# Performance work log

Hardware: AMD Instinct MI355X
Metric: run time of the kernel (lower is better)

Reference implementation:

```python
import jax, jax.numpy as jnp
import numpy as np
from jax import lax

B, DIM, DIM_OUT, NH = 8, 512, 512, 8
HD = DIM_OUT // NH          # 64, also the depthwise-conv channel count
SQ, SKV = (1, 1), (2, 2)    # stride_q, stride_kv
PAD = 1                      # kernel 3 -> padding 3//2
SCALE = HD ** -0.5
EPS = 1e-6


def _dw_conv(x, w, stride):
    # x: [N, C, H, W], w: [C, 1, kh, kw]; depthwise conv (groups = C), no bias
    return lax.conv_general_dilated(
        x, w, window_strides=stride, padding=[(PAD, PAD), (PAD, PAD)],
        dimension_numbers=('NCHW', 'OIHW', 'NCHW'),
        feature_group_count=x.shape[1])


def _ln(x, w, b):
    m = jnp.mean(x, -1, keepdims=True)
    v = jnp.var(x, -1, keepdims=True)
    return (x - m) * lax.rsqrt(v + EPS) * w + b


def _pool(t, w, stride, ln_w, ln_b, H, W):
    # t: [B, NH, 1+H*W, HD] with cls token at index 0
    Bn = t.shape[0]
    cls = t[:, :, :1, :]
    body = t[:, :, 1:, :].reshape(Bn * NH, H, W, HD).transpose(0, 3, 1, 2)
    body = _dw_conv(body, w, stride)
    ph, pw = body.shape[2], body.shape[3]
    body = body.reshape(Bn, NH, HD, ph * pw).transpose(0, 1, 3, 2)
    out = jnp.concatenate([cls, body], axis=2)
    return _ln(out, ln_w, ln_b), (ph, pw)


def _rel_bias(r_q4, q_shape, k_shape, rel_pos_h, rel_pos_w):
    # r_q4: [B, NH, q_h*q_w, HD] (cls token stripped)
    q_h, q_w = q_shape
    k_h, k_w = k_shape

    def dist(qs, ks):
        qr, kr = max(ks / qs, 1.0), max(qs / ks, 1.0)
        d = np.arange(qs)[:, None] * qr - np.arange(ks)[None, :] * kr + (ks - 1) * kr
        return d.astype(np.int64)

    Rh = rel_pos_h[dist(q_h, k_h)]  # [q_h, k_h, HD]
    Rw = rel_pos_w[dist(q_w, k_w)]  # [q_w, k_w, HD]
    r_q = r_q4.reshape(r_q4.shape[0], NH, q_h, q_w, HD)
    rel_h = jnp.einsum('byhwc,hkc->byhwk', r_q, Rh)  # [B,NH,q_h,q_w,k_h]
    rel_w = jnp.einsum('byhwc,wkc->byhwk', r_q, Rw)  # [B,NH,q_h,q_w,k_w]
    return rel_h[..., :, None] + rel_w[..., None, :]  # [B,NH,q_h,q_w,k_h,k_w]


def setup_inputs() -> dict:
    key = jax.random.key(0)
    ks = jax.random.split(key, 16)
    H = W = 56
    N = H * W + 1
    rel_dim = 2 * H - 1  # 111
    return {
        'x': jax.random.normal(ks[0], (B, N, DIM), jnp.float32),
        'qkv_w': jax.random.normal(ks[1], (3 * DIM_OUT, DIM), jnp.float32) * DIM ** -0.5,
        'qkv_b': jax.random.normal(ks[2], (3 * DIM_OUT,), jnp.float32) * 0.02,
        'proj_w': jax.random.normal(ks[3], (DIM_OUT, DIM_OUT), jnp.float32) * DIM_OUT ** -0.5,
        'proj_b': jax.random.normal(ks[4], (DIM_OUT,), jnp.float32) * 0.02,
        'pool_q_w': jax.random.normal(ks[5], (HD, 1, 3, 3), jnp.float32) / 3.0,
        'pool_k_w': jax.random.normal(ks[6], (HD, 1, 3, 3), jnp.float32) / 3.0,
        'pool_v_w': jax.random.normal(ks[7], (HD, 1, 3, 3), jnp.float32) / 3.0,
        'lnq_w': 1.0 + 0.1 * jax.random.normal(ks[8], (HD,), jnp.float32),
        'lnq_b': 0.02 * jax.random.normal(ks[9], (HD,), jnp.float32),
        'lnk_w': 1.0 + 0.1 * jax.random.normal(ks[10], (HD,), jnp.float32),
        'lnk_b': 0.02 * jax.random.normal(ks[11], (HD,), jnp.float32),
        'lnv_w': 1.0 + 0.1 * jax.random.normal(ks[12], (HD,), jnp.float32),
        'lnv_b': 0.02 * jax.random.normal(ks[13], (HD,), jnp.float32),
        'rel_pos_h': 0.02 * jax.random.normal(ks[14], (rel_dim, HD), jnp.float32),
        'rel_pos_w': 0.02 * jax.random.normal(ks[15], (rel_dim, HD), jnp.float32),
        'hw_h': 56,
        'hw_w': 56,
    }


def reference(x, qkv_w, qkv_b, proj_w, proj_b, pool_q_w, pool_k_w, pool_v_w,
              lnq_w, lnq_b, lnk_w, lnk_b, lnv_w, lnv_b, rel_pos_h, rel_pos_w,
              hw_h, hw_w):
    Bn, N, _ = x.shape
    qkv = (x @ qkv_w.T + qkv_b).reshape(Bn, N, 3, NH, HD).transpose(2, 0, 3, 1, 4)
    q, k, v = qkv[0], qkv[1], qkv[2]  # each [B, NH, N, HD]
    q, q_shape = _pool(q, pool_q_w, SQ, lnq_w, lnq_b, hw_h, hw_w)
    k, k_shape = _pool(k, pool_k_w, SKV, lnk_w, lnk_b, hw_h, hw_w)
    v, _ = _pool(v, pool_v_w, SKV, lnv_w, lnv_b, hw_h, hw_w)
    attn = (q * SCALE) @ k.swapaxes(-2, -1)  # [B, NH, Nq, Nk]
    q_h, q_w = q_shape
    k_h, k_w = k_shape
    bias = _rel_bias(q[:, :, 1:, :], q_shape, k_shape, rel_pos_h, rel_pos_w)
    blk = attn[:, :, 1:, 1:].reshape(Bn, NH, q_h, q_w, k_h, k_w) + bias
    attn = attn.at[:, :, 1:, 1:].set(blk.reshape(Bn, NH, q_h * q_w, k_h * k_w))
    attn = jax.nn.softmax(attn, axis=-1)
    out = attn @ v                                   # [B, NH, Nq, HD]
    out = out.at[:, :, 1:, :].add(q[:, :, 1:, :])    # residual on non-cls rows
    out = out.transpose(0, 2, 1, 3).reshape(Bn, -1, DIM_OUT)
    return out @ proj_w.T + proj_b
```

## Files before the change

### kernel.cpp

```cpp
#include <hip/hip_runtime.h>
#include <hip/hip_bf16.h>
#include <cstdint>
#include <cstddef>

#define BB 8
#define NHH 8
#define NQ 3137
#define NKV 785
#define HDIM 64
#define AUG 128
#define MROWS (BB*NQ)
#define SCALE 0.125f
#define VTP 832

typedef unsigned short ushort_t;
typedef __attribute__((ext_vector_type(8))) short s16x8;
typedef __attribute__((ext_vector_type(4))) float f32x4;
typedef __attribute__((ext_vector_type(16))) float f32x16;

__device__ __forceinline__ float bf2f(ushort_t u) {
  union { unsigned int i; float f; } v; v.i = ((unsigned int)u) << 16; return v.f;
}
__device__ __forceinline__ ushort_t f2bf(float f) {
  union { float f; unsigned int i; } v; v.f = f;
  unsigned int r = v.i + 0x7fffu + ((v.i >> 16) & 1u);
  return (ushort_t)(r >> 16);
}
__device__ __forceinline__ unsigned int cvt_pk_bf16(float lo, float hi) {
  unsigned int r;
  asm("v_cvt_pk_bf16_f32 %0, %1, %2" : "=v"(r) : "v"(lo), "v"(hi));
  return r;
}
__device__ __forceinline__ s16x8 lds_frag8(const ushort_t* base, int row, int slot) {
  const char* p = (const char*)base + row * 128 + (((slot ^ (row & 7)) & 7) << 4);
  return *(const s16x8*)p;
}
__device__ __forceinline__ s16x8 lds_frag16(const ushort_t* base, int row, int slot) {
  const char* p = (const char*)base + row * 256 + (((slot ^ (row & 15)) & 15) << 4);
  return *(const s16x8*)p;
}

__global__ __launch_bounds__(256) void cast_bf16_kernel(
    const float* __restrict__ in, ushort_t* __restrict__ outp, int n4) {
  const int i = blockIdx.x * 256 + threadIdx.x;
  if (i >= n4) return;
  const float4 v = ((const float4*)in)[i];
  uint2 o;
  o.x = cvt_pk_bf16(v.x, v.y);
  o.y = cvt_pk_bf16(v.z, v.w);
  *(uint2*)(outp + (size_t)i * 4) = o;
}

template<int EPI>
__global__ __launch_bounds__(256) void mfma_gemm_glds(
    const ushort_t* __restrict__ A, const ushort_t* __restrict__ W,
    const float* __restrict__ bias, void* __restrict__ outp, int M) {
  __shared__ ushort_t As[128 * 64];
  __shared__ ushort_t Bs[128 * 64];
  const int tid = threadIdx.x;
  const int l = tid & 63, w = tid >> 6;
  const int wr = w >> 1, wc = w & 1;
  const int lrow = l & 15, lk = l >> 4;
  const int m0 = blockIdx.y * 128, n0 = blockIdx.x * 128;
  const int lr8 = l >> 3;
  const int swzch = ((l & 7) ^ lr8) * 8;
  f32x4 acc[4][4];
  #pragma unroll
  for (int i = 0; i < 4; ++i) {
    #pragma unroll
    for (int j = 0; j < 4; ++j) acc[i][j] = (f32x4){0.f, 0.f, 0.f, 0.f};
  }
  for (int k0 = 0; k0 < 512; k0 += 64) {
    __syncthreads();
    #pragma unroll
    for (int j = 0; j < 4; ++j) {
      const int rb = (w * 4 + j) * 8 + lr8;
      int mA = m0 + rb; if (mA > M - 1) mA = M - 1;
      const ushort_t* sa = A + (size_t)mA * 512 + k0 + swzch;
      const ushort_t* sb = W + (size_t)(n0 + rb) * 512 + k0 + swzch;
      __builtin_amdgcn_global_load_lds((void*)sa, (void*)(As + (w * 4 + j) * 512), 16, 0, 0);
      __builtin_amdgcn_global_load_lds((void*)sb, (void*)(Bs + (w * 4 + j) * 512), 16, 0, 0);
    }
    __syncthreads();
    #pragma unroll
    for (int sub = 0; sub < 2; ++sub) {
      s16x8 af[4], bfr[4];
      #pragma unroll
      for (int mi = 0; mi < 4; ++mi) {
        const int r = wr * 64 + mi * 16 + lrow;
        const int slot = (sub * 4 + lk) ^ (r & 7);
        af[mi] = *(const s16x8*)(As + r * 64 + slot * 8);
      }
      #pragma unroll
      for (int ni = 0; ni < 4; ++ni) {
        const int r = wc * 64 + ni * 16 + lrow;
        const int slot = (sub * 4 + lk) ^ (r & 7);
        bfr[ni] = *(const s16x8*)(Bs + r * 64 + slot * 8);
      }
      #pragma unroll
      for (int mi = 0; mi < 4; ++mi) {
        #pragma unroll
        for (int ni = 0; ni < 4; ++ni)
          acc[mi][ni] = __builtin_amdgcn_mfma_f32_16x16x32_bf16(
              af[mi], bfr[ni], acc[mi][ni], 0, 0, 0);
      }
    }
  }
  #pragma unroll
  for (int mi = 0; mi < 4; ++mi) {
    #pragma unroll
    for (int r = 0; r < 4; ++r) {
      const int m = m0 + wr * 64 + mi * 16 + 4 * lk + r;
      if (m >= M) continue;
      #pragma unroll
      for (int ni = 0; ni < 4; ++ni) {
        const int n = n0 + wc * 64 + ni * 16 + lrow;
        const float v = acc[mi][ni][r] + bias[n];
        if (EPI == 0) {
          const int which = n >> 9, y = (n >> 6) & 7, c = n & 63;
          const int b_ = m / NQ, tok = m - b_ * NQ;
          ((ushort_t*)outp)[((((size_t)which * BB + b_) * NHH + y) * NQ + tok) * HDIM + c] = f2bf(v);
        } else {
          ((float*)outp)[(size_t)m * 512 + n] = v;
        }
      }
    }
  }
}

template<int MODE>
__global__ __launch_bounds__(256) void pool_ln_kernel(
    const ushort_t* __restrict__ in, ushort_t* __restrict__ out0,
    ushort_t* __restrict__ out1,
    const float* __restrict__ cw, const float* __restrict__ lnw,
    const float* __restrict__ lnb, int stride, int OW, int R) {
  const int tid = threadIdx.x;
  const int c = tid & 63;
  const int rid = blockIdx.x * 4 + (tid >> 6);
  const int by = rid / R;
  const int n = rid - by * R;
  const ushort_t* ibase = in + (size_t)by * NQ * HDIM;
  float val;
  if (n == 0) {
    val = bf2f(ibase[c]);
  } else {
    const int p = n - 1;
    const int ho = p / OW, wo = p - ho * OW;
    float s = 0.f;
    #pragma unroll
    for (int dh = 0; dh < 3; ++dh) {
      const int hh = ho * stride + dh - 1;
      if (hh < 0 || hh >= 56) continue;
      #pragma unroll
      for (int dw = 0; dw < 3; ++dw) {
        const int ww = wo * stride + dw - 1;
        if (ww < 0 || ww >= 56) continue;
        s += cw[c * 9 + dh * 3 + dw] * bf2f(ibase[(size_t)(1 + hh * 56 + ww) * HDIM + c]);
      }
    }
    val = s;
  }
  float sum = val, sq = val * val;
  #pragma unroll
  for (int off = 32; off > 0; off >>= 1) {
    sum += __shfl_xor(sum, off);
    sq  += __shfl_xor(sq,  off);
  }
  const float mean = sum * (1.f / 64.f);
  const float var  = sq * (1.f / 64.f) - mean * mean;
  const float rs = rsqrtf(var + 1e-6f);
  const float lno = (val - mean) * rs * lnw[c] + lnb[c];
  if (MODE == 0) {
    out0[(size_t)rid * HDIM + c] = f2bf(lno);
  } else if (MODE == 1) {
    out0[(size_t)rid * HDIM + c] = f2bf(lno);
    out1[(size_t)rid * AUG + c] = f2bf(lno * SCALE);
    out1[(size_t)rid * AUG + 64 + c] = 0;
  } else {
    out0[(size_t)rid * AUG + c] = f2bf(lno);
    ushort_t aug = 0;
    if (n >= 1) {
      const int p = n - 1;
      const int kh = p / 28, kw = p - 28 * kh;
      if (c < 28) { if (c == kh) aug = 0x3F80; }
      else if (c < 56) { if (c - 28 == kw) aug = 0x3F80; }
    }
    out0[(size_t)rid * AUG + 64 + c] = aug;
  }
}

__global__ __launch_bounds__(256) void transpose_v_kernel(
    const ushort_t* __restrict__ vin, ushort_t* __restrict__ vtout) {
  __shared__ ushort_t T[64][65];
  const int tid = threadIdx.x;
  const int by = blockIdx.y;
  const int n0 = blockIdx.x * 64;
  #pragma unroll
  for (int half = 0; half < 2; ++half) {
    const int idx = tid + half * 256;
    const int r = idx >> 3, s = idx & 7;
    const int n = n0 + r;
    uint4 d = make_uint4(0u, 0u, 0u, 0u);
    if (n < NKV) d = *(const uint4*)(vin + ((size_t)by * NKV + n) * HDIM + s * 8);
    const ushort_t* dp = (const ushort_t*)&d;
    #pragma unroll
    for (int e = 0; e < 8; ++e) T[r][s * 8 + e] = dp[e];
  }
  __syncthreads();
  #pragma unroll
  for (int half = 0; half < 2; ++half) {
    const int idx = tid + half * 256;
    const int c = idx >> 3, g = idx & 7;
    ushort_t pk[8];
    #pragma unroll
    for (int e = 0; e < 8; ++e) pk[e] = T[g * 8 + e][c];
    *(uint4*)(vtout + ((size_t)by * 64 + c) * VTP + n0 + g * 8) = *(const uint4*)pk;
  }
}

__global__ __launch_bounds__(256) void relbias_mfma_kernel(
    const ushort_t* __restrict__ qb, const float* __restrict__ rph,
    const float* __restrict__ rpw, ushort_t* __restrict__ qaug) {
  const int tid = threadIdx.x;
  const int l = tid & 63, w = tid >> 6;
  const int lrow = l & 15, lk = l >> 4;
  const int hw = blockIdx.y;
  const int mode = blockIdx.z;
  const int r0 = blockIdx.x * 256 + w * 64;
  const float* tab = mode ? rpw : rph;
  s16x8 bfr[2][2];
  #pragma unroll
  for (int ni = 0; ni < 2; ++ni) {
    const int kh = ni * 16 + lrow;
    int trow = hw - 2 * kh + 54;
    if (trow < 0) trow = 0;
    const float* tr = tab + (size_t)trow * 64 + lk * 8;
    #pragma unroll
    for (int k0 = 0; k0 < 2; ++k0) {
      const float4 t0 = *(const float4*)(tr + k0 * 32);
      const float4 t1 = *(const float4*)(tr + k0 * 32 + 4);
      s16x8 bb;
      bb[0] = (short)f2bf(t0.x); bb[1] = (short)f2bf(t0.y);
      bb[2] = (short)f2bf(t0.z); bb[3] = (short)f2bf(t0.w);
      bb[4] = (short)f2bf(t1.x); bb[5] = (short)f2bf(t1.y);
      bb[6] = (short)f2bf(t1.z); bb[7] = (short)f2bf(t1.w);
      bfr[ni][k0] = bb;
    }
  }
  s16x8 af[4][2];
  #pragma unroll
  for (int mi = 0; mi < 4; ++mi) {
    const int rA = r0 + mi * 16 + lrow;
    const int by = rA / 56, oth = rA - 56 * by;
    const int tok = mode ? (1 + oth * 56 + hw) : (1 + hw * 56 + oth);
    const ushort_t* qp = qb + ((size_t)by * NQ + tok) * HDIM + lk * 8;
    af[mi][0] = *(const s16x8*)(qp);
    af[mi][1] = *(const s16x8*)(qp + 32);
  }
  f32x4 acc[4][2];
  #pragma unroll
  for (int mi = 0; mi < 4; ++mi) {
    #pragma unroll
    for (int ni = 0; ni < 2; ++ni) acc[mi][ni] = (f32x4){0.f, 0.f, 0.f, 0.f};
  }
  #pragma unroll
  for (int k0 = 0; k0 < 2; ++k0) {
    #pragma unroll
    for (int mi = 0; mi < 4; ++mi) {
      #pragma unroll
      for (int ni = 0; ni < 2; ++ni)
        acc[mi][ni] = __builtin_amdgcn_mfma_f32_16x16x32_bf16(
            af[mi][k0], bfr[ni][k0], acc[mi][ni], 0, 0, 0);
    }
  }
  const int augofs = 64 + mode * 28;
  #pragma unroll
  for (int mi = 0; mi < 4; ++mi) {
    #pragma unroll
    for (int r = 0; r < 4; ++r) {
      const int row = r0 + mi * 16 + 4 * lk + r;
      const int by = row / 56, oth = row - 56 * by;
      const int tok = 1 + (mode ? (oth * 56 + hw) : (hw * 56 + oth));
      ushort_t* orow = qaug + ((size_t)by * NQ + tok) * AUG + augofs;
      #pragma unroll
      for (int ni = 0; ni < 2; ++ni) {
        const int kh = ni * 16 + lrow;
        if (kh < 28) orow[kh] = f2bf(acc[mi][ni][r]);
      }
    }
  }
}

__global__ __launch_bounds__(256) void attn_mfma32_kernel(
    const ushort_t* __restrict__ qaug, const ushort_t* __restrict__ kaug,
    const ushort_t* __restrict__ qb, const ushort_t* __restrict__ vt,
    ushort_t* __restrict__ outp) {
  __shared__ ushort_t Kl[64 * AUG];
  __shared__ ushort_t Vl[64 * 64];
  const int tid = threadIdx.x;
  const int l = tid & 63, w = tid >> 6;
  const int h = l >> 5, q5 = l & 31;
  const int by = blockIdx.y;
  const int qt0 = blockIdx.x * 128;
  const int qloc = w * 32 + q5;
  const int qglob = qt0 + qloc;
  const int qcl = qglob < NQ ? qglob : NQ - 1;
  const ushort_t* qrow = qaug + ((size_t)by * NQ + qcl) * AUG;
  s16x8 qf[8];
  #pragma unroll
  for (int cb = 0; cb < 8; ++cb)
    qf[cb] = *(const s16x8*)(qrow + cb * 16 + h * 8);
  f32x16 ot0, ot1;
  #pragma unroll
  for (int i = 0; i < 16; ++i) { ot0[i] = 0.f; ot1[i] = 0.f; }
  float mr = -1e30f, lr = 0.f;
  const int krow = tid >> 2, ks4 = (tid & 3) * 4;
  const int vrow = tid >> 3, vslot = tid & 7;
  #pragma unroll 1
  for (int it = 0; it < 13; ++it) {
    const int j0 = it * 64;
    int jK = j0 + krow; if (jK > NKV - 1) jK = NKV - 1;
    const ushort_t* ksrc = kaug + ((size_t)by * NKV + jK) * AUG + ks4 * 8;
    const uint4 kd0 = *(const uint4*)(ksrc);
    const uint4 kd1 = *(const uint4*)(ksrc + 8);
    const uint4 kd2 = *(const uint4*)(ksrc + 16);
    const uint4 kd3 = *(const uint4*)(ksrc + 24);
    const uint4 vd0 = *(const uint4*)(vt + ((size_t)by * 64 + vrow) * VTP + j0 + vslot * 8);
    const uint4 vd1 = *(const uint4*)(vt + ((size_t)by * 64 + vrow + 32) * VTP + j0 + vslot * 8);
    __syncthreads();
    {
      char* kbase = (char*)Kl + krow * 256;
      const int rm = krow & 15;
      *(uint4*)(kbase + (((ks4 + 0) ^ rm) << 4)) = kd0;
      *(uint4*)(kbase + (((ks4 + 1) ^ rm) << 4)) = kd1;
      *(uint4*)(kbase + (((ks4 + 2) ^ rm) << 4)) = kd2;
      *(uint4*)(kbase + (((ks4 + 3) ^ rm) << 4)) = kd3;
      *(uint4*)((char*)Vl + vrow * 128 + (((vslot ^ (vrow & 7)) & 7) << 4)) = vd0;
      *(uint4*)((char*)Vl + (vrow + 32) * 128 + (((vslot ^ ((vrow + 32) & 7)) & 7) << 4)) = vd1;
    }
    __syncthreads();
    f32x16 st0, st1;
    #pragma unroll
    for (int i = 0; i < 16; ++i) { st0[i] = 0.f; st1[i] = 0.f; }
    #pragma unroll
    for (int cb = 0; cb < 8; ++cb) {
      st0 = __builtin_amdgcn_mfma_f32_32x32x16_bf16(
          lds_frag16(Kl, q5, cb * 2 + h), qf[cb], st0, 0, 0, 0);
      st1 = __builtin_amdgcn_mfma_f32_32x32x16_bf16(
          lds_frag16(Kl, 32 + q5, cb * 2 + h), qf[cb], st1, 0, 0, 0);
    }
    float pa[16], pb[16];
    #pragma unroll
    for (int r = 0; r < 16; ++r) { pa[r] = st0[r]; pb[r] = st1[r]; }
    if (it == 12) {
      #pragma unroll
      for (int r = 0; r < 16; ++r) {
        const int klocal = (r & 3) + 8 * (r >> 2) + 4 * h;
        if (768 + klocal >= NKV) pa[r] = -1e30f;
        pb[r] = -1e30f;
      }
    }
    float mloc = pa[0];
    #pragma unroll
    for (int r = 1; r < 16; ++r) mloc = fmaxf(mloc, pa[r]);
    #pragma unroll
    for (int r = 0; r < 16; ++r) mloc = fmaxf(mloc, pb[r]);
    mloc = fmaxf(mloc, __shfl_xor(mloc, 32));
    const float mn = fmaxf(mr, mloc);
    const float sc = __expf(mr - mn);
    mr = mn;
    float ps = 0.f;
    #pragma unroll
    for (int r = 0; r < 16; ++r) { pa[r] = __expf(pa[r] - mn); ps += pa[r]; }
    #pragma unroll
    for (int r = 0; r < 16; ++r) { pb[r] = __expf(pb[r] - mn); ps += pb[r]; }
    ps += __shfl_xor(ps, 32);
    lr = lr * sc + ps;
    #pragma unroll
    for (int i = 0; i < 16; ++i) { ot0[i] *= sc; ot1[i] *= sc; }
    auto pvstep = [&](const float (&pv)[16], int kt) {
      #pragma unroll
      for (int kbk = 0; kbk < 2; ++kbk) {
        const unsigned int pk01 = cvt_pk_bf16(pv[kbk * 8 + 0], pv[kbk * 8 + 1]);
        const unsigned int pk23 = cvt_pk_bf16(pv[kbk * 8 + 2], pv[kbk * 8 + 3]);
        const unsigned int pk45 = cvt_pk_bf16(pv[kbk * 8 + 4], pv[kbk * 8 + 5]);
        const unsigned int pk67 = cvt_pk_bf16(pv[kbk * 8 + 6], pv[kbk * 8 + 7]);
        const unsigned int sA = (unsigned int)__shfl_xor((int)pk01, 32);
        const unsigned int sB = (unsigned int)__shfl_xor((int)pk45, 32);
        const unsigned int sC = (unsigned int)__shfl_xor((int)pk23, 32);
        const unsigned int sD = (unsigned int)__shfl_xor((int)pk67, 32);
        int4 fw;
        fw.x = (int)(h ? sB : pk01);
        fw.y = (int)(h ? sD : pk23);
        fw.z = (int)(h ? pk45 : sA);
        fw.w = (int)(h ? pk67 : sC);
        s16x8 pf;
        __builtin_memcpy(&pf, &fw, 16);
        const int slot = kt * 4 + kbk * 2 + h;
        ot0 = __builtin_amdgcn_mfma_f32_32x32x16_bf16(
            lds_frag8(Vl, q5, slot), pf, ot0, 0, 0, 0);
        ot1 = __builtin_amdgcn_mfma_f32_32x32x16_bf16(
            lds_frag8(Vl, 32 + q5, slot), pf, ot1, 0, 0, 0);
      }
    };
    pvstep(pa, 0);
    pvstep(pb, 1);
  }
  const float inv = 1.f / lr;
  if (qglob < NQ) {
    const int b_ = by >> 3, y_ = by & 7;
    ushort_t* obase = outp + ((size_t)b_ * NQ + qglob) * 512 + (size_t)y_ * 64;
    const ushort_t* rbase = qb + ((size_t)by * NQ + qglob) * HDIM;
    #pragma unroll
    for (int ch = 0; ch < 2; ++ch) {
      #pragma unroll
      for (int rg = 0; rg < 4; ++rg) {
        const int c0 = ch * 32 + 8 * rg + 4 * h;
        float vv[4];
        #pragma unroll
        for (int e = 0; e < 4; ++e)
          vv[e] = (ch ? ot1[rg * 4 + e] : ot0[rg * 4 + e]) * inv;
        if (qglob > 0) {
          #pragma unroll
          for (int e = 0; e < 4; ++e) vv[e] += bf2f(rbase[c0 + e]);
        }
        ushort_t pk[4] = { f2bf(vv[0]), f2bf(vv[1]), f2bf(vv[2]), f2bf(vv[3]) };
        *(uint2*)(obase + c0) = *(const uint2*)pk;
      }
    }
  }
}

extern "C" void kernel_launch(void* const* d_in, const int* in_sizes, int n_in,
                              void* d_out, int out_size, void* d_ws, size_t ws_size,
                              hipStream_t stream) {
  const float* x        = (const float*)d_in[0];
  const float* qkv_w    = (const float*)d_in[1];
  const float* qkv_b    = (const float*)d_in[2];
  const float* proj_w   = (const float*)d_in[3];
  const float* proj_b   = (const float*)d_in[4];
  const float* pool_q_w = (const float*)d_in[5];
  const float* pool_k_w = (const float*)d_in[6];
  const float* pool_v_w = (const float*)d_in[7];
  const float* lnq_w    = (const float*)d_in[8];
  const float* lnq_b    = (const float*)d_in[9];
  const float* lnk_w    = (const float*)d_in[10];
  const float* lnk_b    = (const float*)d_in[11];
  const float* lnv_w    = (const float*)d_in[12];
  const float* lnv_b    = (const float*)d_in[13];
  const float* rel_pos_h = (const float*)d_in[14];
  const float* rel_pos_w = (const float*)d_in[15];

  constexpr size_t E1 = (size_t)BB * NHH * NQ * HDIM;
  char* ws = (char*)d_ws;
  size_t off = 0;
  ushort_t* x_bf     = (ushort_t*)(ws + off); off += (size_t)MROWS * 512 * 2;
  ushort_t* qkvw_bf  = (ushort_t*)(ws + off); off += (size_t)1536 * 512 * 2;
  ushort_t* projw_bf = (ushort_t*)(ws + off); off += (size_t)512 * 512 * 2;
  ushort_t* qkv_raw  = (ushort_t*)(ws + off); off += 3 * E1 * 2;
  ushort_t* q_bf     = (ushort_t*)(ws + off); off += E1 * 2;
  ushort_t* qaug     = (ushort_t*)(ws + off); off += (size_t)BB * NHH * NQ * AUG * 2;
  ushort_t* kaug     = (ushort_t*)(ws + off); off += (size_t)BB * NHH * NKV * AUG * 2;
  ushort_t* v_bf     = (ushort_t*)(ws + off); off += (size_t)BB * NHH * NKV * HDIM * 2;
  ushort_t* v_t      = (ushort_t*)(ws + off); off += (size_t)64 * 64 * VTP * 2;
  ushort_t* attn_bf  = qkv_raw;

  cast_bf16_kernel<<<(MROWS * 512 / 4 + 255) / 256, 256, 0, stream>>>(x, x_bf, MROWS * 512 / 4);
  cast_bf16_kernel<<<768, 256, 0, stream>>>(qkv_w, qkvw_bf, 1536 * 512 / 4);
  cast_bf16_kernel<<<256, 256, 0, stream>>>(proj_w, projw_bf, 512 * 512 / 4);

  mfma_gemm_glds<0><<<dim3(12, 197), 256, 0, stream>>>(
      x_bf, qkvw_bf, qkv_b, (void*)qkv_raw, MROWS);

  pool_ln_kernel<1><<<(64 * NQ) / 4,  256, 0, stream>>>(qkv_raw,          q_bf, qaug, pool_q_w, lnq_w, lnq_b, 1, 56, NQ);
  pool_ln_kernel<2><<<(64 * NKV) / 4, 256, 0, stream>>>(qkv_raw + E1,     kaug, nullptr, pool_k_w, lnk_w, lnk_b, 2, 28, NKV);
  pool_ln_kernel<0><<<(64 * NKV) / 4, 256, 0, stream>>>(qkv_raw + 2 * E1, v_bf, nullptr, pool_v_w, lnv_w, lnv_b, 2, 28, NKV);

  transpose_v_kernel<<<dim3(13, 64), 256, 0, stream>>>(v_bf, v_t);

  relbias_mfma_kernel<<<dim3(14, 56, 2), 256, 0, stream>>>(q_bf, rel_pos_h, rel_pos_w, qaug);

  attn_mfma32_kernel<<<dim3(25, 64), 256, 0, stream>>>(qaug, kaug, q_bf, v_t, attn_bf);

  mfma_gemm_glds<1><<<dim3(4, 197), 256, 0, stream>>>(
      attn_bf, projw_bf, proj_b, d_out, MROWS);
}
```

Measured before the change: 447.5 us.

## Double-buffer K/V tiles with direct global-to-LDS loads and lazy softmax rescale

The attention kernel now double-buffers its K and V shared-memory tiles and fills them with global_load_lds, prefetching the next tile while the current one is used. This hides load latency and removes one barrier per iteration. It also adds s_setprio around the MFMA blocks, tree reductions for the row max and sum, and a lazy online-softmax rescale that is skipped while the new max stays within 8 of the running max. The cost is twice the LDS per block, which may lower occupancy, and correctness of the async LDS fill depends on the single barrier at the end of each iteration.

```diff
diff --git a/kernel.cpp b/kernel.cpp
--- a/kernel.cpp
+++ b/kernel.cpp
@@ -295,8 +295,8 @@
     const ushort_t* __restrict__ qaug, const ushort_t* __restrict__ kaug,
     const ushort_t* __restrict__ qb, const ushort_t* __restrict__ vt,
     ushort_t* __restrict__ outp) {
-  __shared__ ushort_t Kl[64 * AUG];
-  __shared__ ushort_t Vl[64 * 64];
+  __shared__ ushort_t Kl[2][64 * 128];
+  __shared__ ushort_t Vl[2][64 * 64];
   const int tid = threadIdx.x;
   const int l = tid & 63, w = tid >> 6;
   const int h = l >> 5, q5 = l & 31;
@@ -314,71 +314,93 @@
   #pragma unroll
   for (int i = 0; i < 16; ++i) { ot0[i] = 0.f; ot1[i] = 0.f; }
   float mr = -1e30f, lr = 0.f;
-  const int krow = tid >> 2, ks4 = (tid & 3) * 4;
-  const int vrow = tid >> 3, vslot = tid & 7;
+  const ushort_t* kab = kaug + (size_t)by * NKV * AUG;
+  const ushort_t* vtb = vt + (size_t)by * 64 * VTP;
+  const int krloc = l >> 4;
+  const int vrloc = l >> 3;
+  auto issue_tile = [&](int it_, int buf) {
+    const int j0 = it_ * 64;
+    ushort_t* Kb = &Kl[buf][0];
+    ushort_t* Vb = &Vl[buf][0];
+    #pragma unroll
+    for (int jj = 0; jj < 4; ++jj) {
+      const int r0 = w * 16 + jj * 4;
+      const int rloc = r0 + krloc;
+      int jg = j0 + rloc; if (jg > NKV - 1) jg = NKV - 1;
+      const int sch = ((l & 15) ^ (rloc & 15)) * 8;
+      const ushort_t* src = kab + (size_t)jg * AUG + sch;
+      __builtin_amdgcn_global_load_lds((void*)src, (void*)(Kb + r0 * 128), 16, 0, 0);
+    }
+    #pragma unroll
+    for (int jj = 0; jj < 2; ++jj) {
+      const int r0 = w * 16 + jj * 8;
+      const int crow = r0 + vrloc;
+      const int sch = ((l & 7) ^ (crow & 7)) * 8;
+      const ushort_t* src = vtb + (size_t)crow * VTP + j0 + sch;
+      __builtin_amdgcn_global_load_lds((void*)src, (void*)(Vb + r0 * 64), 16, 0, 0);
+    }
+  };
+  issue_tile(0, 0);
+  __syncthreads();
   #pragma unroll 1
   for (int it = 0; it < 13; ++it) {
-    const int j0 = it * 64;
-    int jK = j0 + krow; if (jK > NKV - 1) jK = NKV - 1;
-    const ushort_t* ksrc = kaug + ((size_t)by * NKV + jK) * AUG + ks4 * 8;
-    const uint4 kd0 = *(const uint4*)(ksrc);
-    const uint4 kd1 = *(const uint4*)(ksrc + 8);
-    const uint4 kd2 = *(const uint4*)(ksrc + 16);
-    const uint4 kd3 = *(const uint4*)(ksrc + 24);
-    const uint4 vd0 = *(const uint4*)(vt + ((size_t)by * 64 + vrow) * VTP + j0 + vslot * 8);
-    const uint4 vd1 = *(const uint4*)(vt + ((size_t)by * 64 + vrow + 32) * VTP + j0 + vslot * 8);
-    __syncthreads();
-    {
-      char* kbase = (char*)Kl + krow * 256;
-      const int rm = krow & 15;
-      *(uint4*)(kbase + (((ks4 + 0) ^ rm) << 4)) = kd0;
-      *(uint4*)(kbase + (((ks4 + 1) ^ rm) << 4)) = kd1;
-      *(uint4*)(kbase + (((ks4 + 2) ^ rm) << 4)) = kd2;
-      *(uint4*)(kbase + (((ks4 + 3) ^ rm) << 4)) = kd3;
-      *(uint4*)((char*)Vl + vrow * 128 + (((vslot ^ (vrow & 7)) & 7) << 4)) = vd0;
-      *(uint4*)((char*)Vl + (vrow + 32) * 128 + (((vslot ^ ((vrow + 32) & 7)) & 7) << 4)) = vd1;
-    }
-    __syncthreads();
+    const int cur = it & 1;
+    const ushort_t* Kc = &Kl[cur][0];
+    const ushort_t* Vc = &Vl[cur][0];
+    if (it < 12) issue_tile(it + 1, cur ^ 1);
     f32x16 st0, st1;
     #pragma unroll
     for (int i = 0; i < 16; ++i) { st0[i] = 0.f; st1[i] = 0.f; }
+    __builtin_amdgcn_s_setprio(1);
     #pragma unroll
     for (int cb = 0; cb < 8; ++cb) {
       st0 = __builtin_amdgcn_mfma_f32_32x32x16_bf16(
-          lds_frag16(Kl, q5, cb * 2 + h), qf[cb], st0, 0, 0, 0);
+          lds_frag16(Kc, q5, cb * 2 + h), qf[cb], st0, 0, 0, 0);
       st1 = __builtin_amdgcn_mfma_f32_32x32x16_bf16(
-          lds_frag16(Kl, 32 + q5, cb * 2 + h), qf[cb], st1, 0, 0, 0);
-    }
-    float pa[16], pb[16];
-    #pragma unroll
-    for (int r = 0; r < 16; ++r) { pa[r] = st0[r]; pb[r] = st1[r]; }
+          lds_frag16(Kc, 32 + q5, cb * 2 + h), qf[cb], st1, 0, 0, 0);
+    }
+    __builtin_amdgcn_s_setprio(0);
     if (it == 12) {
       #pragma unroll
       for (int r = 0; r < 16; ++r) {
         const int klocal = (r & 3) + 8 * (r >> 2) + 4 * h;
-        if (768 + klocal >= NKV) pa[r] = -1e30f;
-        pb[r] = -1e30f;
-      }
-    }
-    float mloc = pa[0];
-    #pragma unroll
-    for (int r = 1; r < 16; ++r) mloc = fmaxf(mloc, pa[r]);
-    #pragma unroll
-    for (int r = 0; r < 16; ++r) mloc = fmaxf(mloc, pb[r]);
-    mloc = fmaxf(mloc, __shfl_xor(mloc, 32));
-    const float mn = fmaxf(mr, mloc);
-    const float sc = __expf(mr - mn);
-    mr = mn;
-    float ps = 0.f;
-    #pragma unroll
-    for (int r = 0; r < 16; ++r) { pa[r] = __expf(pa[r] - mn); ps += pa[r]; }
-    #pragma unroll
-    for (int r = 0; r < 16; ++r) { pb[r] = __expf(pb[r] - mn); ps += pb[r]; }
-    ps += __shfl_xor(ps, 32);
-    lr = lr * sc + ps;
-    #pragma unroll
-    for (int i = 0; i < 16; ++i) { ot0[i] *= sc; ot1[i] *= sc; }
-    auto pvstep = [&](const float (&pv)[16], int kt) {
+        if (768 + klocal >= NKV) st0[r] = -1e30f;
+        st1[r] = -1e30f;
+      }
+    }
+    float tm[16];
+    #pragma unroll
+    for (int r = 0; r < 16; ++r) tm[r] = fmaxf(st0[r], st1[r]);
+    #pragma unroll
+    for (int s = 8; s > 0; s >>= 1) {
+      #pragma unroll
+      for (int r = 0; r < 8; ++r)
+        if (r < s) tm[r] = fmaxf(tm[r], tm[r + s]);
+    }
+    float mloc = fmaxf(tm[0], __shfl_xor(tm[0], 32));
+    if (!__all(mloc <= mr + 8.f)) {
+      const float mn = fmaxf(mr, mloc);
+      const float sc = __expf(mr - mn);
+      mr = mn;
+      lr *= sc;
+      #pragma unroll
+      for (int i = 0; i < 16; ++i) { ot0[i] *= sc; ot1[i] *= sc; }
+    }
+    float ts[16];
+    #pragma unroll
+    for (int r = 0; r < 16; ++r) {
+      st0[r] = __expf(st0[r] - mr);
+      st1[r] = __expf(st1[r] - mr);
+      ts[r] = st0[r] + st1[r];
+    }
+    #pragma unroll
+    for (int s = 8; s > 0; s >>= 1) {
+      #pragma unroll
+      for (int r = 0; r < 8; ++r)
+        if (r < s) ts[r] += ts[r + s];
+    }
+    lr += ts[0] + __shfl_xor(ts[0], 32);
+    auto pvstep = [&](const f32x16& pv, int kt) {
       #pragma unroll
       for (int kbk = 0; kbk < 2; ++kbk) {
         const unsigned int pk01 = cvt_pk_bf16(pv[kbk * 8 + 0], pv[kbk * 8 + 1]);
@@ -397,14 +419,17 @@
         s16x8 pf;
         __builtin_memcpy(&pf, &fw, 16);
         const int slot = kt * 4 + kbk * 2 + h;
+        __builtin_amdgcn_s_setprio(1);
         ot0 = __builtin_amdgcn_mfma_f32_32x32x16_bf16(
-            lds_frag8(Vl, q5, slot), pf, ot0, 0, 0, 0);
+            lds_frag8(Vc, q5, slot), pf, ot0, 0, 0, 0);
         ot1 = __builtin_amdgcn_mfma_f32_32x32x16_bf16(
-            lds_frag8(Vl, 32 + q5, slot), pf, ot1, 0, 0, 0);
+            lds_frag8(Vc, 32 + q5, slot), pf, ot1, 0, 0, 0);
+        __builtin_amdgcn_s_setprio(0);
       }
     };
-    pvstep(pa, 0);
-    pvstep(pb, 1);
+    pvstep(st0, 0);
+    pvstep(st1, 1);
+    __syncthreads();
   }
   const float inv = 1.f / lr;
   if (qglob < NQ) {
```

Result: no change. 448.0 us (median of 2 runs) (+0.1%).
